# Kernel optimization log

Hardware: AMD Instinct MI355X
Metric: run time of the kernel (lower is better)

## Reference

```python
import jax, jax.numpy as jnp
import numpy as np

B, S, H, K, V = 2, 512, 1024, 4, 32000
EPS_RMS = 1e-5
EPS_LOG = 1e-10

def setup_inputs() -> dict:
    key = jax.random.key(0)
    ks = jax.random.split(key, 7)
    return {
        "hidden_states": jax.random.normal(ks[0], (B, S, H), dtype=jnp.float32),
        "rms_scale": jnp.ones((H,), dtype=jnp.float32),
        "gate_down_w": jax.random.normal(ks[1], (H, H // 2), dtype=jnp.float32) * 0.02,
        "gate_down_b": jnp.zeros((H // 2,), dtype=jnp.float32),
        "gate_up_w": jax.random.normal(ks[2], (H // 2, K), dtype=jnp.float32) * 0.02,
        "gate_up_b": jnp.zeros((K,), dtype=jnp.float32),
        "expert_w": jax.random.normal(ks[3], (H, K * V), dtype=jnp.float32) * 0.02,
    }

def reference(hidden_states, rms_scale, gate_down_w, gate_down_b, gate_up_w, gate_up_b, expert_w):
    # RMSNorm
    x = hidden_states
    var = jnp.mean(jnp.square(x), axis=-1, keepdims=True)
    x = x * jax.lax.rsqrt(var + EPS_RMS) * rms_scale  # (B,S,H)
    # Learned gate: Dense -> silu -> Dense -> softmax over experts
    g = jax.nn.silu(jnp.einsum('bsh,hd->bsd', x, gate_down_w) + gate_down_b)
    gate_logits = jnp.einsum('bsd,dk->bsk', g, gate_up_w) + gate_up_b
    gate_weights = jax.nn.softmax(gate_logits, axis=-1)  # (B,S,K)
    # Expert projections: one big GEMM, reshape to (B,S,K,V)
    logits_all = jnp.einsum('bsh,hv->bsv', x, expert_w).reshape(B, S, K, V)
    expert_probs = jax.nn.softmax(logits_all.astype(jnp.float32), axis=-1)  # (B,S,K,V)
    mixed_probs = jnp.einsum('bsk,bskv->bsv', gate_weights.astype(jnp.float32), expert_probs)
    return jnp.log(mixed_probs + EPS_LOG).astype(hidden_states.dtype)
```

## Files before the change

### kernel.cpp

```cpp
#include <hip/hip_runtime.h>
#include <hip/hip_bf16.h>

#define TOK 1024
#define H 1024
#define NK 4
#define NV 32000
#define NN 128000
#define EPSR 1e-5f
#define EPSL 1e-10f

typedef __attribute__((ext_vector_type(8))) short short8;
typedef __attribute__((ext_vector_type(4))) float float4v;

__global__ __launch_bounds__(256) void k_rmsnorm(const float* __restrict__ hs,
                                                 const float* __restrict__ scale,
                                                 float* __restrict__ xf,
                                                 __hip_bfloat16* __restrict__ xb) {
    int t = blockIdx.x;
    int tid = threadIdx.x;
    int w = tid >> 6, l = tid & 63;
    float4 v = ((const float4*)(hs + (size_t)t * H))[tid];
    float ss = v.x * v.x + v.y * v.y + v.z * v.z + v.w * v.w;
#pragma unroll
    for (int m = 32; m; m >>= 1) ss += __shfl_xor(ss, m);
    __shared__ float red[4];
    if (l == 0) red[w] = ss;
    __syncthreads();
    float tot = red[0] + red[1] + red[2] + red[3];
    float rs = rsqrtf(tot * (1.0f / (float)H) + EPSR);
    float4 sc = ((const float4*)scale)[tid];
    float4 y;
    y.x = v.x * rs * sc.x; y.y = v.y * rs * sc.y;
    y.z = v.z * rs * sc.z; y.w = v.w * rs * sc.w;
    ((float4*)(xf + (size_t)t * H))[tid] = y;
    union { __hip_bfloat162 h; unsigned int u; } p0, p1;
    p0.h = __float22bfloat162_rn(make_float2(y.x, y.y));
    p1.h = __float22bfloat162_rn(make_float2(y.z, y.w));
    uint2 pk; pk.x = p0.u; pk.y = p1.u;
    ((uint2*)(xb + (size_t)t * H))[tid] = pk;
}

__global__ __launch_bounds__(256) void k_gate(const float* __restrict__ xf,
                                              const float* __restrict__ Wgd,
                                              const float* __restrict__ bgd,
                                              const float* __restrict__ Wgu,
                                              const float* __restrict__ bgu,
                                              float* __restrict__ gate_w) {
    __shared__ float xs[8][H];
    __shared__ float gs[8][512];
    int t0 = blockIdx.x * 8;
    int tid = threadIdx.x;
#pragma unroll
    for (int i = 0; i < 8; i++) {
        int idx = i * 256 + tid;
        int r = idx >> 8, c4 = idx & 255;
        *(float4*)&xs[r][c4 * 4] = *(const float4*)&xf[(size_t)(t0 + r) * H + c4 * 4];
    }
    __syncthreads();
    float acc[8][2];
#pragma unroll
    for (int r = 0; r < 8; r++) { acc[r][0] = 0.f; acc[r][1] = 0.f; }
    int d0 = tid, d1 = tid + 256;
    for (int h = 0; h < H; h += 4) {
        float w0[4], w1[4];
#pragma unroll
        for (int j = 0; j < 4; j++) {
            w0[j] = Wgd[(size_t)(h + j) * 512 + d0];
            w1[j] = Wgd[(size_t)(h + j) * 512 + d1];
        }
#pragma unroll
        for (int r = 0; r < 8; r++) {
            float4 xv = *(const float4*)&xs[r][h];
            acc[r][0] += xv.x * w0[0] + xv.y * w0[1] + xv.z * w0[2] + xv.w * w0[3];
            acc[r][1] += xv.x * w1[0] + xv.y * w1[1] + xv.z * w1[2] + xv.w * w1[3];
        }
    }
    float b0 = bgd[d0], b1 = bgd[d1];
#pragma unroll
    for (int r = 0; r < 8; r++) {
        float v0 = acc[r][0] + b0;
        float v1 = acc[r][1] + b1;
        gs[r][d0] = v0 / (1.f + __expf(-v0));
        gs[r][d1] = v1 / (1.f + __expf(-v1));
    }
    __syncthreads();
    int w = tid >> 6, l = tid & 63;
#pragma unroll
    for (int rr = 0; rr < 2; rr++) {
        int r = w * 2 + rr;
        float4 a = make_float4(0.f, 0.f, 0.f, 0.f);
#pragma unroll
        for (int i = 0; i < 8; i++) {
            int d = i * 64 + l;
            float g = gs[r][d];
            float4 wu = *(const float4*)&Wgu[(size_t)d * 4];
            a.x += g * wu.x; a.y += g * wu.y; a.z += g * wu.z; a.w += g * wu.w;
        }
#pragma unroll
        for (int m = 32; m; m >>= 1) {
            a.x += __shfl_xor(a.x, m);
            a.y += __shfl_xor(a.y, m);
            a.z += __shfl_xor(a.z, m);
            a.w += __shfl_xor(a.w, m);
        }
        if (l == 0) {
            float l0 = a.x + bgu[0], l1 = a.y + bgu[1];
            float l2 = a.z + bgu[2], l3 = a.w + bgu[3];
            float mx = fmaxf(fmaxf(l0, l1), fmaxf(l2, l3));
            float e0 = __expf(l0 - mx), e1 = __expf(l1 - mx);
            float e2 = __expf(l2 - mx), e3 = __expf(l3 - mx);
            float s = e0 + e1 + e2 + e3;
            float inv = 1.f / s;
            float4 o = make_float4(e0 * inv, e1 * inv, e2 * inv, e3 * inv);
            *(float4*)&gate_w[(size_t)(t0 + r) * 4] = o;
        }
    }
}

__global__ __launch_bounds__(256) void k_convw(const float* __restrict__ W,
                                               __hip_bfloat16* __restrict__ Wt) {
    __shared__ __align__(8) __hip_bfloat16 T[64][68];
    int n0 = blockIdx.x * 64;
    int k0 = blockIdx.y * 64;
    int tid = threadIdx.x;
#pragma unroll
    for (int i = 0; i < 4; i++) {
        int j = i * 256 + tid;
        int kr = j >> 4;
        int nc4 = (j & 15) * 4;
        float4 v = *(const float4*)&W[(size_t)(k0 + kr) * NN + n0 + nc4];
        union { __hip_bfloat162 h; unsigned int u; } q0, q1;
        q0.h = __float22bfloat162_rn(make_float2(v.x, v.y));
        q1.h = __float22bfloat162_rn(make_float2(v.z, v.w));
        uint2 pk; pk.x = q0.u; pk.y = q1.u;
        *(uint2*)&T[kr][nc4] = pk;
    }
    __syncthreads();
#pragma unroll
    for (int i = 0; i < 2; i++) {
        int j = i * 256 + tid;
        int nr = j >> 3;
        int kc = (j & 7) * 8;
        union { __hip_bfloat16 h[8]; uint4 u; } tp;
#pragma unroll
        for (int q = 0; q < 8; q++) tp.h[q] = T[kc + q][nr];
        *(uint4*)&Wt[(size_t)(n0 + nr) * H + k0 + kc] = tp.u;
    }
}

__global__ __launch_bounds__(256) void k_gemm2(const __hip_bfloat16* __restrict__ xb,
                                               const __hip_bfloat16* __restrict__ Wt,
                                               __hip_bfloat16* __restrict__ E,
                                               float* __restrict__ Z) {
    __shared__ __align__(16) __hip_bfloat16 As[128 * 32];
    __shared__ __align__(16) __hip_bfloat16 Bs[128 * 32];
    int tid = threadIdx.x;
    int tn = blockIdx.x >> 3;
    int tm = blockIdx.x & 7;
    size_t n0 = (size_t)tn * 128;
    int l = tid & 63, w = tid >> 6;
    int wm = w >> 1, wn = w & 1;

    float4v acc[4][4];
#pragma unroll
    for (int i = 0; i < 4; i++)
#pragma unroll
        for (int j = 0; j < 4; j++) acc[i][j] = (float4v){0.f, 0.f, 0.f, 0.f};

    for (int k0 = 0; k0 < H; k0 += 32) {
#pragma unroll
        for (int i = 0; i < 2; i++) {
            int ch = i * 256 + tid;
            int row = ch >> 2, kg = ch & 3;
            const __hip_bfloat16* ga = xb + (size_t)(tm * 128 + row) * H + k0 + kg * 8;
            __builtin_amdgcn_global_load_lds(
                (const __attribute__((address_space(1))) void*)ga,
                (__attribute__((address_space(3))) void*)((char*)As + ch * 16), 16, 0, 0);
            const __hip_bfloat16* gb = Wt + (n0 + row) * H + k0 + kg * 8;
            __builtin_amdgcn_global_load_lds(
                (const __attribute__((address_space(1))) void*)gb,
                (__attribute__((address_space(3))) void*)((char*)Bs + ch * 16), 16, 0, 0);
        }
        __syncthreads();
        short8 a[4], b[4];
#pragma unroll
        for (int mf = 0; mf < 4; mf++)
            a[mf] = *(const short8*)((const char*)As +
                     ((wm * 64 + mf * 16 + (l & 15)) << 6) + ((l >> 4) << 4));
#pragma unroll
        for (int nf = 0; nf < 4; nf++)
            b[nf] = *(const short8*)((const char*)Bs +
                     ((wn * 64 + nf * 16 + (l & 15)) << 6) + ((l >> 4) << 4));
#pragma unroll
        for (int mf = 0; mf < 4; mf++)
#pragma unroll
            for (int nf = 0; nf < 4; nf++)
                acc[mf][nf] = __builtin_amdgcn_mfma_f32_16x16x32_bf16(
                    a[mf], b[nf], acc[mf][nf], 0, 0, 0);
        __syncthreads();
    }

    int kexp = tn / 250;
    int colbase = wn * 64 + (l & 15);
#pragma unroll
    for (int mf = 0; mf < 4; mf++) {
        float zs[4] = {0.f, 0.f, 0.f, 0.f};
#pragma unroll
        for (int nf = 0; nf < 4; nf++) {
#pragma unroll
            for (int r = 0; r < 4; r++) {
                float e = __expf(acc[mf][nf][r]);
                int row = wm * 64 + mf * 16 + ((l >> 4) << 2) + r;
                int token = tm * 128 + row;
                size_t col = n0 + colbase + nf * 16;
                E[(size_t)token * NN + col] = __float2bfloat16(e);
                zs[r] += e;
            }
        }
#pragma unroll
        for (int r = 0; r < 4; r++) {
            float s = zs[r];
            s += __shfl_xor(s, 1);
            s += __shfl_xor(s, 2);
            s += __shfl_xor(s, 4);
            s += __shfl_xor(s, 8);
            if ((l & 15) == 0) {
                int row = wm * 64 + mf * 16 + ((l >> 4) << 2) + r;
                atomicAdd(&Z[(size_t)(tm * 128 + row) * NK + kexp], s);
            }
        }
    }
}

__global__ __launch_bounds__(256) void k_gemm(const __hip_bfloat16* __restrict__ xb,
                                              const float* __restrict__ W,
                                              __hip_bfloat16* __restrict__ E,
                                              float* __restrict__ Z) {
    __shared__ __align__(16) __hip_bfloat16 As[128 * 32];
    __shared__ __align__(16) __hip_bfloat16 Bs[128 * 32];
    int tid = threadIdx.x;
    int tn = blockIdx.x >> 3;
    int tm = blockIdx.x & 7;
    size_t n0 = (size_t)tn * 128;
    int w = tid >> 6, l = tid & 63;
    int wm = w >> 1, wn = w & 1;

    float4v acc[4][4];
#pragma unroll
    for (int i = 0; i < 4; i++)
#pragma unroll
        for (int j = 0; j < 4; j++) acc[i][j] = (float4v){0.f, 0.f, 0.f, 0.f};

    for (int k0 = 0; k0 < H; k0 += 32) {
#pragma unroll
        for (int i = 0; i < 2; i++) {
            int ch = tid + i * 256;
            int row = ch >> 2, kg = ch & 3;
            const __hip_bfloat16* gp = xb + (size_t)(tm * 128 + row) * H + k0 + kg * 8;
            __builtin_amdgcn_global_load_lds(
                (const __attribute__((address_space(1))) void*)gp,
                (__attribute__((address_space(3))) void*)((char*)As + ch * 16), 16, 0, 0);
        }
#pragma unroll
        for (int i = 0; i < 2; i++) {
            int ch = tid + i * 256;
            int n = ch & 127, kg = ch >> 7;
            const float* gp = W + (size_t)(k0 + kg * 8) * NN + n0 + n;
            float f[8];
#pragma unroll
            for (int j = 0; j < 8; j++) f[j] = gp[(size_t)j * NN];
            union { __hip_bfloat162 h; unsigned int u; } q0, q1, q2, q3;
            q0.h = __float22bfloat162_rn(make_float2(f[0], f[1]));
            q1.h = __float22bfloat162_rn(make_float2(f[2], f[3]));
            q2.h = __float22bfloat162_rn(make_float2(f[4], f[5]));
            q3.h = __float22bfloat162_rn(make_float2(f[6], f[7]));
            uint4 pk; pk.x = q0.u; pk.y = q1.u; pk.z = q2.u; pk.w = q3.u;
            int sw = kg ^ ((n >> 1) & 3);
            *(uint4*)((char*)Bs + (n << 6) + (sw << 4)) = pk;
        }
        __syncthreads();
        short8 a[4], b[4];
#pragma unroll
        for (int mf = 0; mf < 4; mf++)
            a[mf] = *(const short8*)((const char*)As +
                     ((wm * 64 + mf * 16 + (l & 15)) << 6) + ((l >> 4) << 4));
#pragma unroll
        for (int nf = 0; nf < 4; nf++) {
            int n = wn * 64 + nf * 16 + (l & 15);
            int sw = (l >> 4) ^ ((n >> 1) & 3);
            b[nf] = *(const short8*)((const char*)Bs + (n << 6) + (sw << 4));
        }
#pragma unroll
        for (int mf = 0; mf < 4; mf++)
#pragma unroll
            for (int nf = 0; nf < 4; nf++)
                acc[mf][nf] = __builtin_amdgcn_mfma_f32_16x16x32_bf16(
                    a[mf], b[nf], acc[mf][nf], 0, 0, 0);
        __syncthreads();
    }

    int kexp = tn / 250;
    int colbase = wn * 64 + (l & 15);
#pragma unroll
    for (int mf = 0; mf < 4; mf++) {
        float zs[4] = {0.f, 0.f, 0.f, 0.f};
#pragma unroll
        for (int nf = 0; nf < 4; nf++) {
#pragma unroll
            for (int r = 0; r < 4; r++) {
                float e = __expf(acc[mf][nf][r]);
                int row = wm * 64 + mf * 16 + ((l >> 4) << 2) + r;
                int token = tm * 128 + row;
                size_t col = n0 + colbase + nf * 16;
                E[(size_t)token * NN + col] = __float2bfloat16(e);
                zs[r] += e;
            }
        }
#pragma unroll
        for (int r = 0; r < 4; r++) {
            float s = zs[r];
            s += __shfl_xor(s, 1);
            s += __shfl_xor(s, 2);
            s += __shfl_xor(s, 4);
            s += __shfl_xor(s, 8);
            if ((l & 15) == 0) {
                int row = wm * 64 + mf * 16 + ((l >> 4) << 2) + r;
                atomicAdd(&Z[(size_t)(tm * 128 + row) * NK + kexp], s);
            }
        }
    }
}

__device__ __forceinline__ float bf_lo(unsigned int u) { return __uint_as_float(u << 16); }
__device__ __forceinline__ float bf_hi(unsigned int u) { return __uint_as_float(u & 0xffff0000u); }

__global__ __launch_bounds__(256) void k_final(const __hip_bfloat16* __restrict__ E,
                                               const float* __restrict__ gw,
                                               const float* __restrict__ Zp,
                                               float* __restrict__ out) {
    int id = blockIdx.x * 256 + threadIdx.x;
    int t = id / 4000;
    int c = id - t * 4000;
    size_t v0 = (size_t)c * 8;
    float4 g = *(const float4*)(gw + (size_t)t * 4);
    float4 z = *(const float4*)(Zp + (size_t)t * 4);
    float c0 = g.x / z.x, c1 = g.y / z.y, c2 = g.z / z.z, c3 = g.w / z.w;
    const __hip_bfloat16* base = E + (size_t)t * NN + v0;
    uint4 e0 = *(const uint4*)(base);
    uint4 e1 = *(const uint4*)(base + NV);
    uint4 e2 = *(const uint4*)(base + 2 * NV);
    uint4 e3 = *(const uint4*)(base + 3 * NV);
    float m[8];
    m[0] = c0 * bf_lo(e0.x) + c1 * bf_lo(e1.x) + c2 * bf_lo(e2.x) + c3 * bf_lo(e3.x);
    m[1] = c0 * bf_hi(e0.x) + c1 * bf_hi(e1.x) + c2 * bf_hi(e2.x) + c3 * bf_hi(e3.x);
    m[2] = c0 * bf_lo(e0.y) + c1 * bf_lo(e1.y) + c2 * bf_lo(e2.y) + c3 * bf_lo(e3.y);
    m[3] = c0 * bf_hi(e0.y) + c1 * bf_hi(e1.y) + c2 * bf_hi(e2.y) + c3 * bf_hi(e3.y);
    m[4] = c0 * bf_lo(e0.z) + c1 * bf_lo(e1.z) + c2 * bf_lo(e2.z) + c3 * bf_lo(e3.z);
    m[5] = c0 * bf_hi(e0.z) + c1 * bf_hi(e1.z) + c2 * bf_hi(e2.z) + c3 * bf_hi(e3.z);
    m[6] = c0 * bf_lo(e0.w) + c1 * bf_lo(e1.w) + c2 * bf_lo(e2.w) + c3 * bf_lo(e3.w);
    m[7] = c0 * bf_hi(e0.w) + c1 * bf_hi(e1.w) + c2 * bf_hi(e2.w) + c3 * bf_hi(e3.w);
    float4 o0, o1;
    o0.x = __logf(m[0] + EPSL); o0.y = __logf(m[1] + EPSL);
    o0.z = __logf(m[2] + EPSL); o0.w = __logf(m[3] + EPSL);
    o1.x = __logf(m[4] + EPSL); o1.y = __logf(m[5] + EPSL);
    o1.z = __logf(m[6] + EPSL); o1.w = __logf(m[7] + EPSL);
    float* op = out + (size_t)t * NV + v0;
    *(float4*)op = o0;
    *(float4*)(op + 4) = o1;
}

extern "C" void kernel_launch(void* const* d_in, const int* in_sizes, int n_in,
                              void* d_out, int out_size, void* d_ws, size_t ws_size,
                              hipStream_t stream) {
    const float* hs  = (const float*)d_in[0];
    const float* rsc = (const float*)d_in[1];
    const float* gdw = (const float*)d_in[2];
    const float* gdb = (const float*)d_in[3];
    const float* guw = (const float*)d_in[4];
    const float* gub = (const float*)d_in[5];
    const float* ew  = (const float*)d_in[6];
    float* out = (float*)d_out;

    char* ws = (char*)d_ws;
    float* xf            = (float*)ws;
    __hip_bfloat16* xb   = (__hip_bfloat16*)(ws + 4194304);
    float* gw            = (float*)(ws + 6291456);
    float* Z             = (float*)(ws + 6307840);

    const size_t NEED_A = 530612224ull;

    k_rmsnorm<<<TOK, 256, 0, stream>>>(hs, rsc, xf, xb);
    k_gate<<<TOK / 8, 256, 0, stream>>>(xf, gdw, gdb, guw, gub, gw);
    hipMemsetAsync(Z, 0, (size_t)TOK * NK * sizeof(float), stream);

    if (ws_size >= NEED_A) {
        __hip_bfloat16* Wt = (__hip_bfloat16*)(ws + 6324224);
        __hip_bfloat16* E  = (__hip_bfloat16*)(ws + 6324224 + 262144000ull);
        k_convw<<<dim3(NN / 64, H / 64), 256, 0, stream>>>(ew, Wt);
        k_gemm2<<<(NN / 128) * (TOK / 128), 256, 0, stream>>>(xb, Wt, E, Z);
        k_final<<<(TOK * (NV / 8)) / 256, 256, 0, stream>>>(E, gw, Z, out);
    } else {
        __hip_bfloat16* E = (__hip_bfloat16*)(ws + 6324224);
        k_gemm<<<(NN / 128) * (TOK / 128), 256, 0, stream>>>(xb, ew, E, Z);
        k_final<<<(TOK * (NV / 8)) / 256, 256, 0, stream>>>(E, gw, Z, out);
    }
}
```

Measured before the change: 1.420 ms.

## Drop weight pre-transpose; fuse fp32 weight conversion into larger-M-tile GEMM

Removes the separate pass that converts and transposes the fp32 expert weight to bf16, and the GEMM that consumed it. The fallback GEMM now converts fp32 weights inside its own tile loop and doubles the M tile to 256 tokens, so each weight tile is read by half as many blocks. The bf16 activations are stored in an XOR-swizzled layout to avoid LDS bank conflicts on A reads. The cost is more accumulator registers and LDS per block, which may lower occupancy, and every block now does the fp32-to-bf16 conversion itself.

```diff
diff --git a/kernel.cpp b/kernel.cpp
--- a/kernel.cpp
+++ b/kernel.cpp
@@ -37,7 +37,9 @@
     p0.h = __float22bfloat162_rn(make_float2(y.x, y.y));
     p1.h = __float22bfloat162_rn(make_float2(y.z, y.w));
     uint2 pk; pk.x = p0.u; pk.y = p1.u;
-    ((uint2*)(xb + (size_t)t * H))[tid] = pk;
+    int c = tid >> 1, hh = tid & 1;
+    int cs = (c & ~3) | ((c & 3) ^ ((t >> 1) & 3));
+    ((uint2*)(xb + (size_t)t * H))[cs * 2 + hh] = pk;
 }
 
 __global__ __launch_bounds__(256) void k_gate(const float* __restrict__ xf,
@@ -117,148 +119,34 @@
     }
 }
 
-__global__ __launch_bounds__(256) void k_convw(const float* __restrict__ W,
-                                               __hip_bfloat16* __restrict__ Wt) {
-    __shared__ __align__(8) __hip_bfloat16 T[64][68];
-    int n0 = blockIdx.x * 64;
-    int k0 = blockIdx.y * 64;
-    int tid = threadIdx.x;
-#pragma unroll
-    for (int i = 0; i < 4; i++) {
-        int j = i * 256 + tid;
-        int kr = j >> 4;
-        int nc4 = (j & 15) * 4;
-        float4 v = *(const float4*)&W[(size_t)(k0 + kr) * NN + n0 + nc4];
-        union { __hip_bfloat162 h; unsigned int u; } q0, q1;
-        q0.h = __float22bfloat162_rn(make_float2(v.x, v.y));
-        q1.h = __float22bfloat162_rn(make_float2(v.z, v.w));
-        uint2 pk; pk.x = q0.u; pk.y = q1.u;
-        *(uint2*)&T[kr][nc4] = pk;
-    }
-    __syncthreads();
-#pragma unroll
-    for (int i = 0; i < 2; i++) {
-        int j = i * 256 + tid;
-        int nr = j >> 3;
-        int kc = (j & 7) * 8;
-        union { __hip_bfloat16 h[8]; uint4 u; } tp;
-#pragma unroll
-        for (int q = 0; q < 8; q++) tp.h[q] = T[kc + q][nr];
-        *(uint4*)&Wt[(size_t)(n0 + nr) * H + k0 + kc] = tp.u;
-    }
-}
-
-__global__ __launch_bounds__(256) void k_gemm2(const __hip_bfloat16* __restrict__ xb,
-                                               const __hip_bfloat16* __restrict__ Wt,
-                                               __hip_bfloat16* __restrict__ E,
-                                               float* __restrict__ Z) {
-    __shared__ __align__(16) __hip_bfloat16 As[128 * 32];
+__global__ __launch_bounds__(256, 2) void k_gemmF(const __hip_bfloat16* __restrict__ xb,
+                                                  const float* __restrict__ W,
+                                                  __hip_bfloat16* __restrict__ E,
+                                                  float* __restrict__ Z) {
+    __shared__ __align__(16) __hip_bfloat16 As[256 * 32];
     __shared__ __align__(16) __hip_bfloat16 Bs[128 * 32];
     int tid = threadIdx.x;
-    int tn = blockIdx.x >> 3;
-    int tm = blockIdx.x & 7;
+    int tn = blockIdx.x >> 2;
+    int tm = blockIdx.x & 2;
+    tm = blockIdx.x & 3;
     size_t n0 = (size_t)tn * 128;
     int l = tid & 63, w = tid >> 6;
     int wm = w >> 1, wn = w & 1;
 
-    float4v acc[4][4];
-#pragma unroll
-    for (int i = 0; i < 4; i++)
+    float4v acc[8][4];
+#pragma unroll
+    for (int i = 0; i < 8; i++)
 #pragma unroll
         for (int j = 0; j < 4; j++) acc[i][j] = (float4v){0.f, 0.f, 0.f, 0.f};
 
     for (int k0 = 0; k0 < H; k0 += 32) {
 #pragma unroll
-        for (int i = 0; i < 2; i++) {
+        for (int i = 0; i < 4; i++) {
             int ch = i * 256 + tid;
             int row = ch >> 2, kg = ch & 3;
-            const __hip_bfloat16* ga = xb + (size_t)(tm * 128 + row) * H + k0 + kg * 8;
+            const __hip_bfloat16* ga = xb + (size_t)(tm * 256 + row) * H + k0 + kg * 8;
             __builtin_amdgcn_global_load_lds(
                 (const __attribute__((address_space(1))) void*)ga,
-                (__attribute__((address_space(3))) void*)((char*)As + ch * 16), 16, 0, 0);
-            const __hip_bfloat16* gb = Wt + (n0 + row) * H + k0 + kg * 8;
-            __builtin_amdgcn_global_load_lds(
-                (const __attribute__((address_space(1))) void*)gb,
-                (__attribute__((address_space(3))) void*)((char*)Bs + ch * 16), 16, 0, 0);
-        }
-        __syncthreads();
-        short8 a[4], b[4];
-#pragma unroll
-        for (int mf = 0; mf < 4; mf++)
-            a[mf] = *(const short8*)((const char*)As +
-                     ((wm * 64 + mf * 16 + (l & 15)) << 6) + ((l >> 4) << 4));
-#pragma unroll
-        for (int nf = 0; nf < 4; nf++)
-            b[nf] = *(const short8*)((const char*)Bs +
-                     ((wn * 64 + nf * 16 + (l & 15)) << 6) + ((l >> 4) << 4));
-#pragma unroll
-        for (int mf = 0; mf < 4; mf++)
-#pragma unroll
-            for (int nf = 0; nf < 4; nf++)
-                acc[mf][nf] = __builtin_amdgcn_mfma_f32_16x16x32_bf16(
-                    a[mf], b[nf], acc[mf][nf], 0, 0, 0);
-        __syncthreads();
-    }
-
-    int kexp = tn / 250;
-    int colbase = wn * 64 + (l & 15);
-#pragma unroll
-    for (int mf = 0; mf < 4; mf++) {
-        float zs[4] = {0.f, 0.f, 0.f, 0.f};
-#pragma unroll
-        for (int nf = 0; nf < 4; nf++) {
-#pragma unroll
-            for (int r = 0; r < 4; r++) {
-                float e = __expf(acc[mf][nf][r]);
-                int row = wm * 64 + mf * 16 + ((l >> 4) << 2) + r;
-                int token = tm * 128 + row;
-                size_t col = n0 + colbase + nf * 16;
-                E[(size_t)token * NN + col] = __float2bfloat16(e);
-                zs[r] += e;
-            }
-        }
-#pragma unroll
-        for (int r = 0; r < 4; r++) {
-            float s = zs[r];
-            s += __shfl_xor(s, 1);
-            s += __shfl_xor(s, 2);
-            s += __shfl_xor(s, 4);
-            s += __shfl_xor(s, 8);
-            if ((l & 15) == 0) {
-                int row = wm * 64 + mf * 16 + ((l >> 4) << 2) + r;
-                atomicAdd(&Z[(size_t)(tm * 128 + row) * NK + kexp], s);
-            }
-        }
-    }
-}
-
-__global__ __launch_bounds__(256) void k_gemm(const __hip_bfloat16* __restrict__ xb,
-                                              const float* __restrict__ W,
-                                              __hip_bfloat16* __restrict__ E,
-                                              float* __restrict__ Z) {
-    __shared__ __align__(16) __hip_bfloat16 As[128 * 32];
-    __shared__ __align__(16) __hip_bfloat16 Bs[128 * 32];
-    int tid = threadIdx.x;
-    int tn = blockIdx.x >> 3;
-    int tm = blockIdx.x & 7;
-    size_t n0 = (size_t)tn * 128;
-    int w = tid >> 6, l = tid & 63;
-    int wm = w >> 1, wn = w & 1;
-
-    float4v acc[4][4];
-#pragma unroll
-    for (int i = 0; i < 4; i++)
-#pragma unroll
-        for (int j = 0; j < 4; j++) acc[i][j] = (float4v){0.f, 0.f, 0.f, 0.f};
-
-    for (int k0 = 0; k0 < H; k0 += 32) {
-#pragma unroll
-        for (int i = 0; i < 2; i++) {
-            int ch = tid + i * 256;
-            int row = ch >> 2, kg = ch & 3;
-            const __hip_bfloat16* gp = xb + (size_t)(tm * 128 + row) * H + k0 + kg * 8;
-            __builtin_amdgcn_global_load_lds(
-                (const __attribute__((address_space(1))) void*)gp,
                 (__attribute__((address_space(3))) void*)((char*)As + ch * 16), 16, 0, 0);
         }
 #pragma unroll
@@ -279,11 +167,13 @@
             *(uint4*)((char*)Bs + (n << 6) + (sw << 4)) = pk;
         }
         __syncthreads();
-        short8 a[4], b[4];
-#pragma unroll
-        for (int mf = 0; mf < 4; mf++)
-            a[mf] = *(const short8*)((const char*)As +
-                     ((wm * 64 + mf * 16 + (l & 15)) << 6) + ((l >> 4) << 4));
+        short8 a[8], b[4];
+#pragma unroll
+        for (int mf = 0; mf < 8; mf++) {
+            int row = wm * 128 + mf * 16 + (l & 15);
+            int sa = (l >> 4) ^ ((row >> 1) & 3);
+            a[mf] = *(const short8*)((const char*)As + (row << 6) + (sa << 4));
+        }
 #pragma unroll
         for (int nf = 0; nf < 4; nf++) {
             int n = wn * 64 + nf * 16 + (l & 15);
@@ -291,7 +181,7 @@
             b[nf] = *(const short8*)((const char*)Bs + (n << 6) + (sw << 4));
         }
 #pragma unroll
-        for (int mf = 0; mf < 4; mf++)
+        for (int mf = 0; mf < 8; mf++)
 #pragma unroll
             for (int nf = 0; nf < 4; nf++)
                 acc[mf][nf] = __builtin_amdgcn_mfma_f32_16x16x32_bf16(
@@ -302,15 +192,15 @@
     int kexp = tn / 250;
     int colbase = wn * 64 + (l & 15);
 #pragma unroll
-    for (int mf = 0; mf < 4; mf++) {
+    for (int mf = 0; mf < 8; mf++) {
         float zs[4] = {0.f, 0.f, 0.f, 0.f};
 #pragma unroll
         for (int nf = 0; nf < 4; nf++) {
 #pragma unroll
             for (int r = 0; r < 4; r++) {
                 float e = __expf(acc[mf][nf][r]);
-                int row = wm * 64 + mf * 16 + ((l >> 4) << 2) + r;
-                int token = tm * 128 + row;
+                int row = wm * 128 + mf * 16 + ((l >> 4) << 2) + r;
+                int token = tm * 256 + row;
                 size_t col = n0 + colbase + nf * 16;
                 E[(size_t)token * NN + col] = __float2bfloat16(e);
                 zs[r] += e;
@@ -324,8 +214,8 @@
             s += __shfl_xor(s, 4);
             s += __shfl_xor(s, 8);
             if ((l & 15) == 0) {
-                int row = wm * 64 + mf * 16 + ((l >> 4) << 2) + r;
-                atomicAdd(&Z[(size_t)(tm * 128 + row) * NK + kexp], s);
+                int row = wm * 128 + mf * 16 + ((l >> 4) << 2) + r;
+                atomicAdd(&Z[(size_t)(tm * 256 + row) * NK + kexp], s);
             }
         }
     }
@@ -386,22 +276,11 @@
     __hip_bfloat16* xb   = (__hip_bfloat16*)(ws + 4194304);
     float* gw            = (float*)(ws + 6291456);
     float* Z             = (float*)(ws + 6307840);
-
-    const size_t NEED_A = 530612224ull;
+    __hip_bfloat16* E    = (__hip_bfloat16*)(ws + 6324224);
 
     k_rmsnorm<<<TOK, 256, 0, stream>>>(hs, rsc, xf, xb);
     k_gate<<<TOK / 8, 256, 0, stream>>>(xf, gdw, gdb, guw, gub, gw);
     hipMemsetAsync(Z, 0, (size_t)TOK * NK * sizeof(float), stream);
-
-    if (ws_size >= NEED_A) {
-        __hip_bfloat16* Wt = (__hip_bfloat16*)(ws + 6324224);
-        __hip_bfloat16* E  = (__hip_bfloat16*)(ws + 6324224 + 262144000ull);
-        k_convw<<<dim3(NN / 64, H / 64), 256, 0, stream>>>(ew, Wt);
-        k_gemm2<<<(NN / 128) * (TOK / 128), 256, 0, stream>>>(xb, Wt, E, Z);
-        k_final<<<(TOK * (NV / 8)) / 256, 256, 0, stream>>>(E, gw, Z, out);
-    } else {
-        __hip_bfloat16* E = (__hip_bfloat16*)(ws + 6324224);
-        k_gemm<<<(NN / 128) * (TOK / 128), 256, 0, stream>>>(xb, ew, E, Z);
-        k_final<<<(TOK * (NV / 8)) / 256, 256, 0, stream>>>(E, gw, Z, out);
-    }
-}
+    k_gemmF<<<(NN / 128) * (TOK / 256), 256, 0, stream>>>(xb, ew, E, Z);
+    k_final<<<(TOK * (NV / 8)) / 256, 256, 0, stream>>>(E, gw, Z, out);
+}
```

New measurement: 1.407 ms. Within noise of the previous version (-0.9%).
